# Kernel optimization log

Measured on AMD Instinct MI355X. Metric: run time of the kernel, lower is better.

The kernel has to match this reference:

```python
import jax, jax.numpy as jnp
import numpy as np

BUCKETS = 16


def conv2d(x, w, b):
    # x: [N, Cin, H, W], w: [Cout, Cin, kh, kw], stride 1, padding 1
    y = jax.lax.conv_general_dilated(
        x, w, window_strides=(1, 1), padding=((1, 1), (1, 1)),
        dimension_numbers=("NCHW", "OIHW", "NCHW"))
    return y + b[None, :, None, None]


def setup_inputs() -> dict:
    key = jax.random.key(0)
    k1, k2, k3, k4, k5 = jax.random.split(key, 5)
    x = jax.random.normal(k1, (32, 64, 112, 112), dtype=jnp.float32)
    W = jax.random.normal(k2, (128, 64, 3, 3), dtype=jnp.float32) * 0.05
    b = jax.random.normal(k3, (128,), dtype=jnp.float32) * 0.05
    b2 = jax.random.normal(k4, (128,), dtype=jnp.float32) * 0.05  # hashed_conv's own bias
    hashed_weights = jax.random.normal(k5, (BUCKETS,), dtype=jnp.float32)
    return {"x": x, "W": W, "b": b, "b2": b2, "hashed_weights": hashed_weights}


def reference(x, W, b, b2, hashed_weights):
    out = conv2d(x, W, b)
    # thresholds derived from min/max of the ORIGINAL weights
    wmax = jnp.max(W)
    wmin = jnp.min(W)
    step = (wmax - wmin) / BUCKETS
    # sequential per-bucket replacement (faithful to in-place loop semantics:
    # values replaced at bucket i are re-compared against later thresholds)
    hw = W
    for i in range(BUCKETS):
        thr = (i + 1) * step + wmin
        hw = jnp.where(hw > thr, hashed_weights[i], hw)
    hashed_out = conv2d(x, hw, b2)
    return (out, hashed_out)
```

## Files before the change

### kernel.cpp

```cpp
#include <hip/hip_runtime.h>
#include <stdint.h>

#define CIN 64
#define HHW 112
#define NPIX 12544
#define COUT 128
#define KTOT 576
#define NBUCKETS 16

typedef __attribute__((ext_vector_type(8))) short s8v;
typedef __attribute__((ext_vector_type(4))) float f4v;
typedef __attribute__((ext_vector_type(8))) unsigned short u8v;

__device__ __forceinline__ unsigned short f2bf(float f) {
  unsigned int u = __float_as_uint(f);
  unsigned int r = (u + 0x7fffu + ((u >> 16) & 1u)) >> 16;
  return (unsigned short)r;
}

__device__ __forceinline__ void gload_lds16(const void* g, void* l) {
  __builtin_amdgcn_global_load_lds(
      (const __attribute__((address_space(1))) unsigned int*)g,
      (__attribute__((address_space(3))) unsigned int*)l, 16, 0, 0);
}

__global__ __launch_bounds__(1024) void hashedconv_prep_kernel(
    const float* __restrict__ W, const float* __restrict__ hashed_w,
    unsigned short* __restrict__ W2, unsigned short* __restrict__ zp) {
  const int NW = COUT * CIN * 9;
  int tid = threadIdx.x;
  if (zp && tid < 128) zp[tid] = 0;
  float vmin = 1e30f, vmax = -1e30f;
  for (int i = tid; i < NW; i += 1024) {
    float v = W[i];
    vmin = fminf(vmin, v);
    vmax = fmaxf(vmax, v);
  }
  #pragma unroll
  for (int off = 32; off > 0; off >>= 1) {
    vmin = fminf(vmin, __shfl_down(vmin, off, 64));
    vmax = fmaxf(vmax, __shfl_down(vmax, off, 64));
  }
  __shared__ float smin[16], smax[16];
  __shared__ float s_wmin, s_step;
  __shared__ float hv[NBUCKETS];
  int wave = tid >> 6, lane = tid & 63;
  if (lane == 0) { smin[wave] = vmin; smax[wave] = vmax; }
  if (tid < NBUCKETS) hv[tid] = hashed_w[tid];
  __syncthreads();
  if (tid == 0) {
    float m = smin[0], M = smax[0];
    #pragma unroll
    for (int i = 1; i < 16; ++i) { m = fminf(m, smin[i]); M = fmaxf(M, smax[i]); }
    s_wmin = m;
    s_step = (M - m) / (float)NBUCKETS;
  }
  __syncthreads();
  float wmin = s_wmin, step = s_step;
  for (int i = tid; i < NW; i += 1024) {
    float v = W[i];
    int co  = i / 576;
    int rem = i - co * 576;
    int cin = rem / 9;
    int off = rem - cin * 9;
    float h = v;
    #pragma unroll
    for (int b = 0; b < NBUCKETS; ++b) {
      float thr = (float)(b + 1) * step + wmin;
      if (h > thr) h = hv[b];
    }
    int oidx = co * KTOT + off * 64 + cin;
    W2[oidx]               = f2bf(v);
    W2[COUT * KTOT + oidx] = f2bf(h);
  }
}

__global__ __launch_bounds__(256) void xpose_kernel(
    const float* __restrict__ x, unsigned short* __restrict__ xb) {
  __shared__ unsigned short t[64][264];
  const int n = blockIdx.y, p0 = blockIdx.x * 256, tid = threadIdx.x;
  const float* xp = x + (size_t)n * CIN * NPIX + p0;
  #pragma unroll
  for (int c = 0; c < 64; ++c)
    t[c][tid] = f2bf(xp[(size_t)c * NPIX + tid]);
  __syncthreads();
  unsigned short* ob = xb + ((size_t)n * NPIX + p0) * 64;
  #pragma unroll
  for (int it = 0; it < 8; ++it) {
    int u = it * 256 + tid;
    int px = u >> 3, slot = u & 7;
    u8v v;
    #pragma unroll
    for (int k = 0; k < 8; ++k) v[k] = t[slot * 8 + k][px];
    *(u8v*)(ob + (size_t)u * 8) = v;
  }
}

#define XS_SHORTS (180 * 64)
#define HALF_SHORTS (128 * 32)

__global__ __launch_bounds__(256, 3) void hashedconv_mfma_kernel(
    const unsigned short* __restrict__ xb, const unsigned short* __restrict__ W2,
    const float* __restrict__ b, const float* __restrict__ b2,
    const unsigned short* __restrict__ zp, float* __restrict__ out,
    size_t out_half) {
  __shared__ __attribute__((aligned(16))) short lds[XS_SHORTS + 3 * HALF_SHORTS];
  short* xs = lds;
  short* ring = lds + XS_SHORTS;

  const int tid = threadIdx.x;
  const int bx = blockIdx.x;
  const int n  = blockIdx.y;
  const int hf = blockIdx.z;
  const int ty = bx / 7, tx = bx - ty * 7;
  const int h0 = ty * 8, w0 = tx * 16;
  const int lane = tid & 63, wv = tid >> 6;
  const int wr = wv >> 1;
  const int wcn = wv & 1;
  const int lrow = lane & 15, g = lane >> 4;

  const unsigned short* Wh = W2 + (size_t)hf * COUT * KTOT;

  #pragma unroll
  for (int it = 0; it < 6; ++it) {
    int u = it * 256 + tid;
    if (u < 1440) {
      int pix = u >> 3, slot = u & 7;
      int py = pix / 18, px = pix - py * 18;
      int gh = h0 - 1 + py, gw = w0 - 1 + px;
      bool inb = (gh >= 0) & (gh < HHW) & (gw >= 0) & (gw < HHW);
      int srcslot = slot ^ (pix & 7);
      const unsigned short* gsrc = inb
          ? xb + (((size_t)n * NPIX + gh * HHW + gw) * 64 + srcslot * 8)
          : zp + srcslot * 8;
      gload_lds16(gsrc, xs + (size_t)u * 8 - (size_t)(lane * 8));
    }
  }

  auto stage_half = [&](int h) {
    short* buf = ring + (size_t)(h % 3) * HALF_SHORTS;
    const unsigned short* src = Wh + (h >> 1) * 64 + (h & 1) * 32;
    #pragma unroll
    for (int j = 0; j < 2; ++j) {
      int u = j * 256 + tid;
      int row = u >> 2, slot = u & 3;
      int srcs = slot ^ ((row >> 2) & 3);
      gload_lds16(src + (size_t)row * KTOT + srcs * 8,
                  buf + (size_t)(j * 256 + wv * 64) * 8);
    }
  };
  stage_half(0);
  stage_half(1);

  f4v acc[4][4];
  #pragma unroll
  for (int i = 0; i < 4; ++i)
    #pragma unroll
    for (int j = 0; j < 4; ++j) acc[i][j] = (f4v)(0.f);

  int sbase[4];
  #pragma unroll
  for (int nt = 0; nt < 4; ++nt) {
    int p = wcn * 64 + nt * 16 + lrow;
    sbase[nt] = (p >> 4) * 18 + (p & 15);
  }

#define PHASE(h_, VM)                                                        \
  {                                                                          \
    asm volatile("s_waitcnt vmcnt(" #VM ")" ::: "memory");                   \
    __builtin_amdgcn_s_barrier();                                            \
    const int h = (h_);                                                      \
    if (h + 2 <= 17) stage_half(h + 2);                                      \
    const short* wbuf = ring + (size_t)(h % 3) * HALF_SHORTS;                \
    const int ch = h >> 1;                                                   \
    const int dh = ch / 3, dw = ch - dh * 3;                                 \
    const int kofs = (h & 1) * 32 + g * 8;                                   \
    s8v af[4], bfv[4];                                                       \
    _Pragma("unroll") for (int mt = 0; mt < 4; ++mt) {                       \
      int row = wr * 64 + mt * 16 + lrow;                                    \
      af[mt] = *(const s8v*)(wbuf + row * 32 + (g ^ ((row >> 2) & 3)) * 8);  \
    }                                                                        \
    _Pragma("unroll") for (int nt = 0; nt < 4; ++nt) {                       \
      int s = sbase[nt] + dh * 18 + dw;                                      \
      bfv[nt] = *(const s8v*)(xs + s * 64 + (kofs ^ ((s & 7) << 3)));        \
    }                                                                        \
    asm volatile("s_waitcnt lgkmcnt(0)" ::: "memory");                       \
    __builtin_amdgcn_sched_barrier(0);                                       \
    __builtin_amdgcn_s_setprio(1);                                           \
    _Pragma("unroll") for (int mt = 0; mt < 4; ++mt)                         \
      _Pragma("unroll") for (int nt = 0; nt < 4; ++nt)                       \
        acc[mt][nt] = __builtin_amdgcn_mfma_f32_16x16x32_bf16(               \
            af[mt], bfv[nt], acc[mt][nt], 0, 0, 0);                          \
    __builtin_amdgcn_s_setprio(0);                                           \
    __builtin_amdgcn_sched_barrier(0);                                       \
  }

  for (int c = 0; c < 8; ++c) {
    PHASE(2 * c, 2);
    PHASE(2 * c + 1, 2);
  }
  PHASE(16, 2);
  PHASE(17, 0);
#undef PHASE

  const float* bias = hf ? b2 : b;
  float* obase = out + (size_t)hf * out_half + (size_t)n * COUT * NPIX;
  #pragma unroll
  for (int mt = 0; mt < 4; ++mt) {
    #pragma unroll
    for (int r = 0; r < 4; ++r) {
      int co = wr * 64 + mt * 16 + g * 4 + r;
      float bv = bias[co];
      #pragma unroll
      for (int nt = 0; nt < 4; ++nt) {
        int p = wcn * 64 + nt * 16 + lrow;
        int h = h0 + (p >> 4), w = w0 + (p & 15);
        obase[(size_t)co * NPIX + h * HHW + w] = acc[mt][nt][r] + bv;
      }
    }
  }
}

__global__ __launch_bounds__(256) void hashedconv_fb_kernel(
    const float* __restrict__ x, const unsigned short* __restrict__ W2,
    const float* __restrict__ b, const float* __restrict__ b2,
    float* __restrict__ out, size_t out_half) {
  __shared__ __attribute__((aligned(16))) short lds[11520 + 8192];
  short* xs = lds;
  short* wcs = lds + 11520;
  const int tid = threadIdx.x;
  const int bx = blockIdx.x;
  const int n  = blockIdx.y;
  const int hf = blockIdx.z;
  const int ty = bx / 7, tx = bx - ty * 7;
  const int h0 = ty * 8, w0 = tx * 16;
  const int lane = tid & 63, wv = tid >> 6;
  const int wr = wv >> 1, wcn = wv & 1;
  const int lrow = lane & 15, g = lane >> 4;
  f4v acc[4][4];
  #pragma unroll
  for (int i = 0; i < 4; ++i)
    #pragma unroll
    for (int j = 0; j < 4; ++j) acc[i][j] = (f4v)(0.f);
  const float* xn = x + (size_t)n * CIN * NPIX;
  for (int u = tid; u < 1440; u += 256) {
    int cg = u / 180;
    int pix = u - cg * 180;
    int pyp = pix / 18, pxp = pix - pyp * 18;
    int gh = h0 - 1 + pyp, gw = w0 - 1 + pxp;
    bool inb = (gh >= 0) & (gh < HHW) & (gw >= 0) & (gw < HHW);
    const float* xp = xn + (size_t)(cg * 8) * NPIX + gh * HHW + gw;
    s8v pk;
    #pragma unroll
    for (int cc = 0; cc < 8; ++cc) {
      float v = inb ? xp[(size_t)cc * NPIX] : 0.f;
      pk[cc] = (short)f2bf(v);
    }
    *(s8v*)(xs + pix * 64 + ((cg * 8) ^ ((pix & 7) << 3))) = pk;
  }
  const unsigned short* Wh = W2 + (size_t)hf * COUT * KTOT;
  for (int c = 0; c < 9; ++c) {
    #pragma unroll
    for (int j = 0; j < 4; ++j) {
      int u = tid + j * 256;
      int row = u >> 3, slot = u & 7;
      s8v v = *(const s8v*)(Wh + (size_t)row * KTOT + c * 64 + slot * 8);
      *(s8v*)(wcs + row * 64 + ((slot * 8) ^ ((row & 7) << 3))) = v;
    }
    __syncthreads();
    int dh = c / 3, dw = c - dh * 3;
    #pragma unroll
    for (int kh2 = 0; kh2 < 2; ++kh2) {
      int kofs = kh2 * 32 + g * 8;
      s8v af[4], bfv[4];
      #pragma unroll
      for (int mt = 0; mt < 4; ++mt) {
        int row = wr * 64 + mt * 16 + lrow;
        af[mt] = *(const s8v*)(wcs + row * 64 + (kofs ^ ((row & 7) << 3)));
      }
      #pragma unroll
      for (int nt = 0; nt < 4; ++nt) {
        int p = wcn * 64 + nt * 16 + lrow;
        int s = ((p >> 4) + dh) * 18 + ((p & 15) + dw);
        bfv[nt] = *(const s8v*)(xs + s * 64 + (kofs ^ ((s & 7) << 3)));
      }
      #pragma unroll
      for (int mt = 0; mt < 4; ++mt)
        #pragma unroll
        for (int nt = 0; nt < 4; ++nt)
          acc[mt][nt] = __builtin_amdgcn_mfma_f32_16x16x32_bf16(
              af[mt], bfv[nt], acc[mt][nt], 0, 0, 0);
    }
    __syncthreads();
  }
  const float* bias = hf ? b2 : b;
  float* obase = out + (size_t)hf * out_half + (size_t)n * COUT * NPIX;
  #pragma unroll
  for (int mt = 0; mt < 4; ++mt) {
    #pragma unroll
    for (int r = 0; r < 4; ++r) {
      int co = wr * 64 + mt * 16 + g * 4 + r;
      float bv = bias[co];
      #pragma unroll
      for (int nt = 0; nt < 4; ++nt) {
        int p = wcn * 64 + nt * 16 + lrow;
        int h = h0 + (p >> 4), w = w0 + (p & 15);
        obase[(size_t)co * NPIX + h * HHW + w] = acc[mt][nt][r] + bv;
      }
    }
  }
}

extern "C" void kernel_launch(void* const* d_in, const int* in_sizes, int n_in,
                              void* d_out, int out_size, void* d_ws, size_t ws_size,
                              hipStream_t stream) {
  const float* x      = (const float*)d_in[0];
  const float* W      = (const float*)d_in[1];
  const float* b      = (const float*)d_in[2];
  const float* b2     = (const float*)d_in[3];
  const float* hashed = (const float*)d_in[4];
  float* out = (float*)d_out;

  const int N = in_sizes[0] / (CIN * NPIX);
  const size_t out_half = (size_t)N * COUT * NPIX;
  const size_t XB_SHORTS = (size_t)N * NPIX * 64;
  const size_t need = (XB_SHORTS + 2 * COUT * KTOT) * 2 + 256;

  if (ws_size >= need) {
    unsigned short* xb = (unsigned short*)d_ws;
    unsigned short* W2 = xb + XB_SHORTS;
    unsigned short* zp = W2 + 2 * COUT * KTOT;
    hipLaunchKernelGGL(hashedconv_prep_kernel, dim3(1), dim3(1024), 0, stream,
                       W, hashed, W2, zp);
    hipLaunchKernelGGL(xpose_kernel, dim3(NPIX / 256, N), dim3(256), 0, stream,
                       x, xb);
    hipLaunchKernelGGL(hashedconv_mfma_kernel, dim3(98, N, 2), dim3(256), 0,
                       stream, xb, W2, b, b2, zp, out, out_half);
  } else {
    unsigned short* W2 = (unsigned short*)d_ws;
    hipLaunchKernelGGL(hashedconv_prep_kernel, dim3(1), dim3(1024), 0, stream,
                       W, hashed, W2, (unsigned short*)nullptr);
    hipLaunchKernelGGL(hashedconv_fb_kernel, dim3(98, N, 2), dim3(256), 0,
                       stream, x, W2, b, b2, out, out_half);
  }
}
```

Measured before the change: 265.3 us.

## Read weight fragments directly from global memory in MFMA-ready layout, drop LDS weight ring

The prep kernel now writes weights in a per-phase, per-output-channel layout so each lane's 8-element MFMA A fragment sits contiguously in global memory. The main kernel drops the triple-buffered LDS weight ring and its per-phase barriers, loading A fragments straight from global/L2 while only the input tile stays in LDS. The grid interleaves the two weight halves along x so neighbouring blocks share the input tile in cache. This shrinks LDS use and removes sync, but exposes global-load latency inside the MFMA loop and loses the explicit prefetch schedule.

```diff
diff --git a/kernel.cpp b/kernel.cpp
--- a/kernel.cpp
+++ b/kernel.cpp
@@ -7,6 +7,7 @@
 #define COUT 128
 #define KTOT 576
 #define NBUCKETS 16
+#define W3_HALF 73728
 
 typedef __attribute__((ext_vector_type(8))) short s8v;
 typedef __attribute__((ext_vector_type(4))) float f4v;
@@ -26,7 +27,7 @@
 
 __global__ __launch_bounds__(1024) void hashedconv_prep_kernel(
     const float* __restrict__ W, const float* __restrict__ hashed_w,
-    unsigned short* __restrict__ W2, unsigned short* __restrict__ zp) {
+    unsigned short* __restrict__ W3, unsigned short* __restrict__ zp) {
   const int NW = COUT * CIN * 9;
   int tid = threadIdx.x;
   if (zp && tid < 128) zp[tid] = 0;
@@ -63,15 +64,18 @@
     int rem = i - co * 576;
     int cin = rem / 9;
     int off = rem - cin * 9;
-    float h = v;
-    #pragma unroll
-    for (int b = 0; b < NBUCKETS; ++b) {
-      float thr = (float)(b + 1) * step + wmin;
-      if (h > thr) h = hv[b];
-    }
-    int oidx = co * KTOT + off * 64 + cin;
-    W2[oidx]               = f2bf(v);
-    W2[COUT * KTOT + oidx] = f2bf(h);
+    float hval = v;
+    #pragma unroll
+    for (int bb = 0; bb < NBUCKETS; ++bb) {
+      float thr = (float)(bb + 1) * step + wmin;
+      if (hval > thr) hval = hv[bb];
+    }
+    int ph = off * 2 + (cin >> 5);
+    int gg = (cin >> 3) & 3;
+    int ee = cin & 7;
+    int oidx = (ph * 128 + co) * 32 + gg * 8 + ee;
+    W3[oidx]           = f2bf(v);
+    W3[W3_HALF + oidx] = f2bf(hval);
   }
 }
 
@@ -97,29 +101,25 @@
 }
 
 #define XS_SHORTS (180 * 64)
-#define HALF_SHORTS (128 * 32)
 
 __global__ __launch_bounds__(256, 3) void hashedconv_mfma_kernel(
-    const unsigned short* __restrict__ xb, const unsigned short* __restrict__ W2,
+    const unsigned short* __restrict__ xb, const unsigned short* __restrict__ W3,
     const float* __restrict__ b, const float* __restrict__ b2,
     const unsigned short* __restrict__ zp, float* __restrict__ out,
     size_t out_half) {
-  __shared__ __attribute__((aligned(16))) short lds[XS_SHORTS + 3 * HALF_SHORTS];
-  short* xs = lds;
-  short* ring = lds + XS_SHORTS;
+  __shared__ __attribute__((aligned(16))) short xs[XS_SHORTS];
 
   const int tid = threadIdx.x;
-  const int bx = blockIdx.x;
-  const int n  = blockIdx.y;
-  const int hf = blockIdx.z;
+  const int bxz = blockIdx.x;
+  const int hf  = bxz & 1;
+  const int bx  = bxz >> 1;
+  const int n   = blockIdx.y;
   const int ty = bx / 7, tx = bx - ty * 7;
   const int h0 = ty * 8, w0 = tx * 16;
   const int lane = tid & 63, wv = tid >> 6;
   const int wr = wv >> 1;
   const int wcn = wv & 1;
   const int lrow = lane & 15, g = lane >> 4;
-
-  const unsigned short* Wh = W2 + (size_t)hf * COUT * KTOT;
 
   #pragma unroll
   for (int it = 0; it < 6; ++it) {
@@ -136,21 +136,7 @@
       gload_lds16(gsrc, xs + (size_t)u * 8 - (size_t)(lane * 8));
     }
   }
-
-  auto stage_half = [&](int h) {
-    short* buf = ring + (size_t)(h % 3) * HALF_SHORTS;
-    const unsigned short* src = Wh + (h >> 1) * 64 + (h & 1) * 32;
-    #pragma unroll
-    for (int j = 0; j < 2; ++j) {
-      int u = j * 256 + tid;
-      int row = u >> 2, slot = u & 3;
-      int srcs = slot ^ ((row >> 2) & 3);
-      gload_lds16(src + (size_t)row * KTOT + srcs * 8,
-                  buf + (size_t)(j * 256 + wv * 64) * 8);
-    }
-  };
-  stage_half(0);
-  stage_half(1);
+  __syncthreads();
 
   f4v acc[4][4];
   #pragma unroll
@@ -165,43 +151,30 @@
     sbase[nt] = (p >> 4) * 18 + (p & 15);
   }
 
-#define PHASE(h_, VM)                                                        \
-  {                                                                          \
-    asm volatile("s_waitcnt vmcnt(" #VM ")" ::: "memory");                   \
-    __builtin_amdgcn_s_barrier();                                            \
-    const int h = (h_);                                                      \
-    if (h + 2 <= 17) stage_half(h + 2);                                      \
-    const short* wbuf = ring + (size_t)(h % 3) * HALF_SHORTS;                \
-    const int ch = h >> 1;                                                   \
-    const int dh = ch / 3, dw = ch - dh * 3;                                 \
-    const int kofs = (h & 1) * 32 + g * 8;                                   \
-    s8v af[4], bfv[4];                                                       \
-    _Pragma("unroll") for (int mt = 0; mt < 4; ++mt) {                       \
-      int row = wr * 64 + mt * 16 + lrow;                                    \
-      af[mt] = *(const s8v*)(wbuf + row * 32 + (g ^ ((row >> 2) & 3)) * 8);  \
-    }                                                                        \
-    _Pragma("unroll") for (int nt = 0; nt < 4; ++nt) {                       \
-      int s = sbase[nt] + dh * 18 + dw;                                      \
-      bfv[nt] = *(const s8v*)(xs + s * 64 + (kofs ^ ((s & 7) << 3)));        \
-    }                                                                        \
-    asm volatile("s_waitcnt lgkmcnt(0)" ::: "memory");                       \
-    __builtin_amdgcn_sched_barrier(0);                                       \
-    __builtin_amdgcn_s_setprio(1);                                           \
-    _Pragma("unroll") for (int mt = 0; mt < 4; ++mt)                         \
-      _Pragma("unroll") for (int nt = 0; nt < 4; ++nt)                       \
-        acc[mt][nt] = __builtin_amdgcn_mfma_f32_16x16x32_bf16(               \
-            af[mt], bfv[nt], acc[mt][nt], 0, 0, 0);                          \
-    __builtin_amdgcn_s_setprio(0);                                           \
-    __builtin_amdgcn_sched_barrier(0);                                       \
-  }
-
-  for (int c = 0; c < 8; ++c) {
-    PHASE(2 * c, 2);
-    PHASE(2 * c + 1, 2);
-  }
-  PHASE(16, 2);
-  PHASE(17, 0);
-#undef PHASE
+  const unsigned short* Wl =
+      W3 + (size_t)hf * W3_HALF + (size_t)(wr * 64 + lrow) * 32 + g * 8;
+
+  #pragma unroll
+  for (int h = 0; h < 18; ++h) {
+    const int ch = h >> 1;
+    const int dh = ch / 3, dw = ch - dh * 3;
+    const int kofs = (h & 1) * 32 + g * 8;
+    s8v af[4], bfv[4];
+    #pragma unroll
+    for (int mt = 0; mt < 4; ++mt)
+      af[mt] = *(const s8v*)(Wl + (size_t)(h * 128 + mt * 16) * 32);
+    #pragma unroll
+    for (int nt = 0; nt < 4; ++nt) {
+      int s = sbase[nt] + dh * 18 + dw;
+      bfv[nt] = *(const s8v*)(xs + s * 64 + (kofs ^ ((s & 7) << 3)));
+    }
+    #pragma unroll
+    for (int mt = 0; mt < 4; ++mt)
+      #pragma unroll
+      for (int nt = 0; nt < 4; ++nt)
+        acc[mt][nt] = __builtin_amdgcn_mfma_f32_16x16x32_bf16(
+            af[mt], bfv[nt], acc[mt][nt], 0, 0, 0);
+  }
 
   const float* bias = hf ? b2 : b;
   float* obase = out + (size_t)hf * out_half + (size_t)n * COUT * NPIX;
@@ -222,7 +195,7 @@
 }
 
 __global__ __launch_bounds__(256) void hashedconv_fb_kernel(
-    const float* __restrict__ x, const unsigned short* __restrict__ W2,
+    const float* __restrict__ x, const unsigned short* __restrict__ W3,
     const float* __restrict__ b, const float* __restrict__ b2,
     float* __restrict__ out, size_t out_half) {
   __shared__ __attribute__((aligned(16))) short lds[11520 + 8192];
@@ -258,13 +231,14 @@
     }
     *(s8v*)(xs + pix * 64 + ((cg * 8) ^ ((pix & 7) << 3))) = pk;
   }
-  const unsigned short* Wh = W2 + (size_t)hf * COUT * KTOT;
+  const unsigned short* Wh = W3 + (size_t)hf * W3_HALF;
   for (int c = 0; c < 9; ++c) {
     #pragma unroll
     for (int j = 0; j < 4; ++j) {
       int u = tid + j * 256;
       int row = u >> 3, slot = u & 7;
-      s8v v = *(const s8v*)(Wh + (size_t)row * KTOT + c * 64 + slot * 8);
+      s8v v = *(const s8v*)(Wh + ((size_t)(c * 2 + (slot >> 2)) * 128 + row) * 32
+                               + (slot & 3) * 8);
       *(s8v*)(wcs + row * 64 + ((slot * 8) ^ ((row & 7) << 3))) = v;
     }
     __syncthreads();
@@ -324,23 +298,23 @@
   const int N = in_sizes[0] / (CIN * NPIX);
   const size_t out_half = (size_t)N * COUT * NPIX;
   const size_t XB_SHORTS = (size_t)N * NPIX * 64;
-  const size_t need = (XB_SHORTS + 2 * COUT * KTOT) * 2 + 256;
+  const size_t need = (XB_SHORTS + 2 * W3_HALF) * 2 + 256;
 
   if (ws_size >= need) {
     unsigned short* xb = (unsigned short*)d_ws;
-    unsigned short* W2 = xb + XB_SHORTS;
-    unsigned short* zp = W2 + 2 * COUT * KTOT;
+    unsigned short* W3 = xb + XB_SHORTS;
+    unsigned short* zp = W3 + 2 * W3_HALF;
     hipLaunchKernelGGL(hashedconv_prep_kernel, dim3(1), dim3(1024), 0, stream,
-                       W, hashed, W2, zp);
+                       W, hashed, W3, zp);
     hipLaunchKernelGGL(xpose_kernel, dim3(NPIX / 256, N), dim3(256), 0, stream,
                        x, xb);
-    hipLaunchKernelGGL(hashedconv_mfma_kernel, dim3(98, N, 2), dim3(256), 0,
-                       stream, xb, W2, b, b2, zp, out, out_half);
+    hipLaunchKernelGGL(hashedconv_mfma_kernel, dim3(196, N), dim3(256), 0,
+                       stream, xb, W3, b, b2, zp, out, out_half);
   } else {
-    unsigned short* W2 = (unsigned short*)d_ws;
+    unsigned short* W3 = (unsigned short*)d_ws;
     hipLaunchKernelGGL(hashedconv_prep_kernel, dim3(1), dim3(1024), 0, stream,
-                       W, hashed, W2, (unsigned short*)nullptr);
+                       W, hashed, W3, (unsigned short*)nullptr);
     hipLaunchKernelGGL(hashedconv_fb_kernel, dim3(98, N, 2), dim3(256), 0,
-                       stream, x, W2, b, b2, out, out_half);
-  }
-}
+                       stream, x, W3, b, b2, out, out_half);
+  }
+}
```

After: 357.0 us. 1.35x slower.
